# Performance work log

Hardware: AMD Instinct MI355X
Metric: run time of the kernel (lower is better)

The kernel has to match this reference:

```python
import jax, jax.numpy as jnp
import numpy as np

N_MELS = 80
FORMANT_START, FORMANT_END = 10, 50
W_L1, W_DELTA, W_DELTA2, W_SC, W_BAND, FORMANT_W = 1.0, 0.5, 0.25, 0.5, 1.0, 2.0
EPS = 1e-8


def _masked_mean(x, mask):
    # mask broadcasts to x's shape; count = sum of the broadcast mask
    n = jnp.maximum(jnp.sum(jnp.broadcast_to(mask, x.shape)), 1.0)
    return jnp.sum(x * mask) / n


def setup_inputs() -> dict:
    key = jax.random.key(0)
    k1, k2, k3 = jax.random.split(key, 3)
    B, T, D = 64, 4000, N_MELS
    pred_mel = jax.random.normal(k1, (B, T, D), dtype=jnp.float32)
    target_mel = jax.random.normal(k2, (B, T, D), dtype=jnp.float32)
    lengths = jax.random.randint(k3, (B,), T // 2, T + 1)
    mel_mask = (jnp.arange(T)[None, :] < lengths[:, None]).astype(jnp.float32)
    band_weights = jnp.ones((D,), dtype=jnp.float32).at[FORMANT_START:FORMANT_END].set(FORMANT_W)
    return {"pred_mel": pred_mel, "target_mel": target_mel, "mel_mask": mel_mask,
            "band_weights": band_weights}


def reference(pred_mel, target_mel, mel_mask, band_weights):
    mask3 = mel_mask[:, :, None]                      # (B,T,1)

    l1 = jnp.abs(pred_mel - target_mel)               # (B,T,D)
    l1_loss = _masked_mean(l1, mask3)

    # 1st-order deltas
    dp = pred_mel[:, 1:] - pred_mel[:, :-1]
    dt = target_mel[:, 1:] - target_mel[:, :-1]
    dmask = (mel_mask[:, 1:] * mel_mask[:, :-1])[:, :, None]
    delta_loss = _masked_mean(jnp.abs(dp - dt), dmask)

    # 2nd-order deltas
    d2p = dp[:, 1:] - dp[:, :-1]
    d2t = dt[:, 1:] - dt[:, :-1]
    d2mask = (mel_mask[:, 2:] * mel_mask[:, 1:-1] * mel_mask[:, :-2])[:, :, None]
    delta2_loss = _masked_mean(jnp.abs(d2p - d2t), d2mask)

    # spectral convergence
    diff = (pred_mel - target_mel) * mask3
    tgt_m = target_mel * mask3
    n = jnp.maximum(jnp.sum(jnp.broadcast_to(mask3, pred_mel.shape)), 1.0)
    sc_num = jnp.sqrt(jnp.sum(diff * diff) / n)
    sc_den = jnp.maximum(jnp.sqrt(jnp.sum(tgt_m * tgt_m) / n), EPS)
    sc_loss = sc_num / sc_den

    # band-weighted L1
    w = band_weights[None, None, :]
    band_loss = _masked_mean(l1 * w, mask3) / jnp.mean(band_weights)

    # energy (per-frame mean over mel bins)
    e_l1 = jnp.abs(pred_mel.mean(axis=-1) - target_mel.mean(axis=-1))  # (B,T)
    energy_loss = _masked_mean(e_l1, mel_mask)

    return (W_L1 * l1_loss + W_DELTA * delta_loss + W_DELTA2 * delta2_loss
            + W_SC * sc_loss + W_BAND * band_loss + 0.5 * energy_loss)
```

## Files before the change

### kernel.cpp

```cpp
#include <hip/hip_runtime.h>
#include <math.h>

#define D_MELS 80
#define T_DIM  4000
#define NQ     10
#define NTHR   256
#define RPI    14


__global__ __launch_bounds__(NTHR) void mel_loss_main(
    const float* __restrict__ pred, const float* __restrict__ tgt,
    const float* __restrict__ mask,
    float* __restrict__ partial, int BT, int Jtot, int K, int nblk)
{
    const int tid  = threadIdx.x;
    const int lane = tid & 63;
    const int qtr  = lane & 3;
    const int rw   = lane >> 2;
    const int gw   = blockIdx.x * (NTHR / 64) + (tid >> 6);

    const float4* p4 = (const float4*)pred;
    const float4* q4 = (const float4*)tgt;

    const int lsrc4 = (lane - 4) & 63;
    const int lsrc8 = (lane - 8) & 63;

    float4 sel0 = make_float4(0.f, 0.f, 0.f, 0.f);
    float4 sel3 = make_float4(0.f, 0.f, 0.f, 0.f);
    if (qtr == 2)      { sel0.z = 1.f; sel0.w = 1.f; }
    else if (qtr == 3) { sel0.x = 1.f; sel0.y = 1.f; sel0.z = 1.f; sel0.w = 1.f; }
    if (qtr == 0)      { sel3.x = 1.f; sel3.y = 1.f; }

    float v_l1 = 0.f, v_band = 0.f, v_diff2 = 0.f, v_tgt2 = 0.f, v_energy = 0.f;
    float v_m = 0.f, v_d = 0.f, v_dm = 0.f, v_d2 = 0.f, v_d2m = 0.f;

    const int j0 = gw * K;
    const int j1 = (j0 + K < Jtot) ? (j0 + K) : Jtot;

    for (int j = j0; j < j1; ++j) {
        const int r = j * RPI - 2 + rw;
        int rload = r;
        if (rload < 0) rload = 0;
        if (rload >= BT) rload = BT - 1;

        float mload = mask[rload];

        if (__any(mload != 0.0f)) {
            const int t = rload % T_DIM;

            const float4* pr = p4 + (size_t)rload * (D_MELS / 4) + qtr;
            const float4* qr = q4 + (size_t)rload * (D_MELS / 4) + qtr;

            float m1 = __shfl(mload, lsrc4, 64);
            float m2 = __shfl(mload, lsrc8, 64);

            const bool contrib = (rw >= 2) && (r < BT);
            float mt   = contrib ? mload : 0.f;
            float dmv  = (t >= 1) ? mt * m1 : 0.f;
            float d2mv = (t >= 2) ? dmv * m2 : 0.f;

            float l1r = 0.f, frr = 0.f, sqr = 0.f, t2r = 0.f, er = 0.f, dr = 0.f, d2r = 0.f;

            #pragma unroll
            for (int k = 0; k < 5; ++k) {
                float4 p = pr[4 * k];
                float4 q = qr[4 * k];
                float e0 = p.x - q.x, e1 = p.y - q.y, e2 = p.z - q.z, e3 = p.w - q.w;

                float f0 = __shfl(e0, lsrc4, 64);
                float f1 = __shfl(e1, lsrc4, 64);
                float f2 = __shfl(e2, lsrc4, 64);
                float f3 = __shfl(e3, lsrc4, 64);
                float g0 = __shfl(e0, lsrc8, 64);
                float g1 = __shfl(e1, lsrc8, 64);
                float g2 = __shfl(e2, lsrc8, 64);
                float g3 = __shfl(e3, lsrc8, 64);

                float a0 = fabsf(e0), a1 = fabsf(e1), a2 = fabsf(e2), a3 = fabsf(e3);
                float ak = a0 + a1 + a2 + a3;
                l1r += ak;
                if (k == 1 || k == 2)      frr += ak;
                else if (k == 0)           frr += a0 * sel0.x + a1 * sel0.y + a2 * sel0.z + a3 * sel0.w;
                else if (k == 3)           frr += a0 * sel3.x + a1 * sel3.y + a2 * sel3.z + a3 * sel3.w;

                sqr += e0 * e0 + e1 * e1 + e2 * e2 + e3 * e3;
                t2r += q.x * q.x + q.y * q.y + q.z * q.z + q.w * q.w;
                er  += e0 + e1 + e2 + e3;
                dr  += fabsf(e0 - f0) + fabsf(e1 - f1) + fabsf(e2 - f2) + fabsf(e3 - f3);
                d2r += fabsf(e0 - 2.f * f0 + g0) + fabsf(e1 - 2.f * f1 + g1)
                     + fabsf(e2 - 2.f * f2 + g2) + fabsf(e3 - 2.f * f3 + g3);
            }

            v_l1    += l1r * mt;
            v_band  += (l1r + frr) * mt;
            v_diff2 += sqr * mt;
            v_tgt2  += t2r * mt;
            v_d     += dr * dmv;
            v_d2    += d2r * d2mv;

            er += __shfl_xor(er, 1, 64);
            er += __shfl_xor(er, 2, 64);
            if (qtr == 0) {
                v_energy += fabsf(er) * mt;
                v_m   += mt;
                v_dm  += dmv;
                v_d2m += d2mv;
            }
        }
    }

    float vals[NQ] = {v_l1, v_band, v_diff2, v_tgt2, v_energy,
                      v_m, v_d, v_dm, v_d2, v_d2m};
    #pragma unroll
    for (int q = 0; q < NQ; ++q) {
        float v = vals[q];
        #pragma unroll
        for (int off = 32; off > 0; off >>= 1)
            v += __shfl_down(v, off, 64);
        vals[q] = v;
    }
    __shared__ float red[NTHR / 64][NQ];
    int wave = tid >> 6;
    if (lane == 0) {
        #pragma unroll
        for (int q = 0; q < NQ; ++q) red[wave][q] = vals[q];
    }
    __syncthreads();
    if (tid < NQ) {
        float s = 0.f;
        #pragma unroll
        for (int wv2 = 0; wv2 < NTHR / 64; ++wv2) s += red[wv2][tid];
        partial[tid * nblk + blockIdx.x] = s;
    }
}

__global__ __launch_bounds__(640) void mel_loss_finalize(
    const float* __restrict__ partial, const float* __restrict__ w,
    float* __restrict__ out, int nblk)
{
    const int tid = threadIdx.x;
    const int wv  = tid >> 6;
    const int lane = tid & 63;
    __shared__ float fin[NQ];

    float s = 0.f;
    for (int i = lane; i < nblk; i += 64) s += partial[wv * nblk + i];
    #pragma unroll
    for (int off = 32; off > 0; off >>= 1) s += __shfl_down(s, off, 64);
    if (lane == 0 && wv < NQ) fin[wv] = s;
    __syncthreads();

    if (tid == 0) {
        float l1s = fin[0], bands = fin[1], diff2 = fin[2], tgt2 = fin[3];
        float energys = fin[4], ms = fin[5], ds = fin[6], dms = fin[7];
        float d2s = fin[8], d2ms = fin[9];

        float wsum = 0.f;
        for (int d = 0; d < D_MELS; ++d) wsum += w[d];
        float wmean = wsum / (float)D_MELS;

        float n1  = fmaxf(ms   * (float)D_MELS, 1.f);
        float nd  = fmaxf(dms  * (float)D_MELS, 1.f);
        float nd2 = fmaxf(d2ms * (float)D_MELS, 1.f);

        float l1_loss     = l1s / n1;
        float delta_loss  = ds / nd;
        float delta2_loss = d2s / nd2;
        float sc_num = sqrtf(diff2 / n1);
        float sc_den = fmaxf(sqrtf(tgt2 / n1), 1e-8f);
        float sc_loss = sc_num / sc_den;
        float band_loss = (bands / n1) / wmean;
        float energy_loss = (energys / (float)D_MELS) / fmaxf(ms, 1.f);

        out[0] = 1.0f * l1_loss + 0.5f * delta_loss + 0.25f * delta2_loss
               + 0.5f * sc_loss + 1.0f * band_loss + 0.5f * energy_loss;
    }
}

extern "C" void kernel_launch(void* const* d_in, const int* in_sizes, int n_in,
                              void* d_out, int out_size, void* d_ws, size_t ws_size,
                              hipStream_t stream) {
    const float* pred = (const float*)d_in[0];
    const float* tgt  = (const float*)d_in[1];
    const float* mask = (const float*)d_in[2];
    const float* w    = (const float*)d_in[3];
    int BT = in_sizes[2];
    float* partial = (float*)d_ws;

    int Jtot = (BT + RPI - 1) / RPI;
    int K = 2;
    int nwaves = (Jtot + K - 1) / K;
    int grid = (nwaves + (NTHR / 64) - 1) / (NTHR / 64);
    while ((size_t)NQ * (size_t)grid * sizeof(float) > ws_size && K < Jtot) {
        K *= 2;
        nwaves = (Jtot + K - 1) / K;
        grid = (nwaves + (NTHR / 64) - 1) / (NTHR / 64);
    }

    mel_loss_main<<<grid, NTHR, 0, stream>>>(pred, tgt, mask, partial, BT, Jtot, K, grid);
    mel_loss_finalize<<<1, 640, 0, stream>>>(partial, w, (float*)d_out, grid);
}
```

Baseline: 189.6 us.

## Double-buffer row-group loads with compile-time tile count per wave

Each wave now processes a fixed six row-groups, with masks preloaded and two register buffers so the loads for group s+2 are issued while group s is computed. This is meant to hide global memory latency in the memory-bound reduction by keeping more loads in flight per wave. It raises register pressure and drops the workspace-size check that used to grow K when the partial buffer was too small, so a small workspace could overflow.

```diff
diff --git a/kernel.cpp b/kernel.cpp
--- a/kernel.cpp
+++ b/kernel.cpp
@@ -6,12 +6,13 @@
 #define NQ     10
 #define NTHR   256
 #define RPI    14
+#define KK     6
 
 
 __global__ __launch_bounds__(NTHR) void mel_loss_main(
     const float* __restrict__ pred, const float* __restrict__ tgt,
     const float* __restrict__ mask,
-    float* __restrict__ partial, int BT, int Jtot, int K, int nblk)
+    float* __restrict__ partial, int BT, int Jtot, int nblk)
 {
     const int tid  = threadIdx.x;
     const int lane = tid & 63;
@@ -21,90 +22,114 @@
 
     const float4* p4 = (const float4*)pred;
     const float4* q4 = (const float4*)tgt;
-
     const int lsrc4 = (lane - 4) & 63;
     const int lsrc8 = (lane - 8) & 63;
 
-    float4 sel0 = make_float4(0.f, 0.f, 0.f, 0.f);
-    float4 sel3 = make_float4(0.f, 0.f, 0.f, 0.f);
-    if (qtr == 2)      { sel0.z = 1.f; sel0.w = 1.f; }
-    else if (qtr == 3) { sel0.x = 1.f; sel0.y = 1.f; sel0.z = 1.f; sel0.w = 1.f; }
-    if (qtr == 0)      { sel3.x = 1.f; sel3.y = 1.f; }
-
     float v_l1 = 0.f, v_band = 0.f, v_diff2 = 0.f, v_tgt2 = 0.f, v_energy = 0.f;
     float v_m = 0.f, v_d = 0.f, v_dm = 0.f, v_d2 = 0.f, v_d2m = 0.f;
 
-    const int j0 = gw * K;
-    const int j1 = (j0 + K < Jtot) ? (j0 + K) : Jtot;
-
-    for (int j = j0; j < j1; ++j) {
-        const int r = j * RPI - 2 + rw;
-        int rload = r;
-        if (rload < 0) rload = 0;
-        if (rload >= BT) rload = BT - 1;
-
-        float mload = mask[rload];
-
-        if (__any(mload != 0.0f)) {
-            const int t = rload % T_DIM;
-
-            const float4* pr = p4 + (size_t)rload * (D_MELS / 4) + qtr;
-            const float4* qr = q4 + (size_t)rload * (D_MELS / 4) + qtr;
-
-            float m1 = __shfl(mload, lsrc4, 64);
-            float m2 = __shfl(mload, lsrc8, 64);
-
-            const bool contrib = (rw >= 2) && (r < BT);
-            float mt   = contrib ? mload : 0.f;
-            float dmv  = (t >= 1) ? mt * m1 : 0.f;
-            float d2mv = (t >= 2) ? dmv * m2 : 0.f;
-
-            float l1r = 0.f, frr = 0.f, sqr = 0.f, t2r = 0.f, er = 0.f, dr = 0.f, d2r = 0.f;
-
-            #pragma unroll
-            for (int k = 0; k < 5; ++k) {
-                float4 p = pr[4 * k];
-                float4 q = qr[4 * k];
-                float e0 = p.x - q.x, e1 = p.y - q.y, e2 = p.z - q.z, e3 = p.w - q.w;
-
-                float f0 = __shfl(e0, lsrc4, 64);
-                float f1 = __shfl(e1, lsrc4, 64);
-                float f2 = __shfl(e2, lsrc4, 64);
-                float f3 = __shfl(e3, lsrc4, 64);
-                float g0 = __shfl(e0, lsrc8, 64);
-                float g1 = __shfl(e1, lsrc8, 64);
-                float g2 = __shfl(e2, lsrc8, 64);
-                float g3 = __shfl(e3, lsrc8, 64);
-
-                float a0 = fabsf(e0), a1 = fabsf(e1), a2 = fabsf(e2), a3 = fabsf(e3);
-                float ak = a0 + a1 + a2 + a3;
-                l1r += ak;
-                if (k == 1 || k == 2)      frr += ak;
-                else if (k == 0)           frr += a0 * sel0.x + a1 * sel0.y + a2 * sel0.z + a3 * sel0.w;
-                else if (k == 3)           frr += a0 * sel3.x + a1 * sel3.y + a2 * sel3.z + a3 * sel3.w;
-
-                sqr += e0 * e0 + e1 * e1 + e2 * e2 + e3 * e3;
-                t2r += q.x * q.x + q.y * q.y + q.z * q.z + q.w * q.w;
-                er  += e0 + e1 + e2 + e3;
-                dr  += fabsf(e0 - f0) + fabsf(e1 - f1) + fabsf(e2 - f2) + fabsf(e3 - f3);
-                d2r += fabsf(e0 - 2.f * f0 + g0) + fabsf(e1 - 2.f * f1 + g1)
-                     + fabsf(e2 - 2.f * f2 + g2) + fabsf(e3 - 2.f * f3 + g3);
-            }
-
-            v_l1    += l1r * mt;
-            v_band  += (l1r + frr) * mt;
-            v_diff2 += sqr * mt;
-            v_tgt2  += t2r * mt;
-            v_d     += dr * dmv;
-            v_d2    += d2r * d2mv;
-
-            er += __shfl_xor(er, 1, 64);
-            er += __shfl_xor(er, 2, 64);
-            if (qtr == 0) {
-                v_energy += fabsf(er) * mt;
-                v_m   += mt;
-                v_dm  += dmv;
-                v_d2m += d2mv;
+    const int j0 = gw * KK;
+
+    auto laneRow = [&](int s) -> int {
+        int r = (j0 + s) * RPI - 2 + rw;
+        return r < 0 ? 0 : (r >= BT ? BT - 1 : r);
+    };
+
+    float mv[KK];
+    #pragma unroll
+    for (int s = 0; s < KK; ++s)
+        mv[s] = (j0 + s < Jtot) ? mask[laneRow(s)] : 0.f;
+
+    float4 PA[5], QA[5], PB[5], QB[5];
+
+    auto issueA = [&](int s) {
+        const int rload = laneRow(s);
+        const float4* pr = p4 + (size_t)rload * (D_MELS / 4) + qtr;
+        const float4* qr = q4 + (size_t)rload * (D_MELS / 4) + qtr;
+        #pragma unroll
+        for (int k = 0; k < 5; ++k) { PA[k] = pr[4 * k]; QA[k] = qr[4 * k]; }
+    };
+    auto issueB = [&](int s) {
+        const int rload = laneRow(s);
+        const float4* pr = p4 + (size_t)rload * (D_MELS / 4) + qtr;
+        const float4* qr = q4 + (size_t)rload * (D_MELS / 4) + qtr;
+        #pragma unroll
+        for (int k = 0; k < 5; ++k) { PB[k] = pr[4 * k]; QB[k] = qr[4 * k]; }
+    };
+
+    auto computeT = [&](const float4 (&P)[5], const float4 (&Q)[5], int s) {
+        const int r = (j0 + s) * RPI - 2 + rw;
+        const int rload = r < 0 ? 0 : (r >= BT ? BT - 1 : r);
+        const int t = rload % T_DIM;
+        const float mload = mv[s];
+        const float m1 = __shfl(mload, lsrc4, 64);
+        const float m2 = __shfl(mload, lsrc8, 64);
+        const bool contrib = (rw >= 2) && (r < BT);
+        const float mt   = contrib ? mload : 0.f;
+        const float dmv  = (t >= 1) ? mt * m1 : 0.f;
+        const float d2mv = (t >= 2) ? dmv * m2 : 0.f;
+
+        float l1r = 0.f, frr = 0.f, sqr = 0.f, t2r = 0.f, er = 0.f, dr = 0.f, d2r = 0.f;
+        #pragma unroll
+        for (int k = 0; k < 5; ++k) {
+            float4 p = P[k], q = Q[k];
+            float e0 = p.x - q.x, e1 = p.y - q.y, e2 = p.z - q.z, e3 = p.w - q.w;
+
+            float f0 = __shfl(e0, lsrc4, 64);
+            float f1 = __shfl(e1, lsrc4, 64);
+            float f2 = __shfl(e2, lsrc4, 64);
+            float f3 = __shfl(e3, lsrc4, 64);
+            float g0 = __shfl(e0, lsrc8, 64);
+            float g1 = __shfl(e1, lsrc8, 64);
+            float g2 = __shfl(e2, lsrc8, 64);
+            float g3 = __shfl(e3, lsrc8, 64);
+
+            float a0 = fabsf(e0), a1 = fabsf(e1), a2 = fabsf(e2), a3 = fabsf(e3);
+            float ak = a0 + a1 + a2 + a3;
+            l1r += ak;
+            if (k == 1 || k == 2) frr += ak;
+            else if (k == 0)      frr += (qtr == 2) ? (a2 + a3) : ((qtr == 3) ? ak : 0.f);
+            else if (k == 3)      frr += (qtr == 0) ? (a0 + a1) : 0.f;
+
+            sqr += e0 * e0 + e1 * e1 + e2 * e2 + e3 * e3;
+            t2r += q.x * q.x + q.y * q.y + q.z * q.z + q.w * q.w;
+            er  += e0 + e1 + e2 + e3;
+            dr  += fabsf(e0 - f0) + fabsf(e1 - f1) + fabsf(e2 - f2) + fabsf(e3 - f3);
+            d2r += fabsf(e0 - 2.f * f0 + g0) + fabsf(e1 - 2.f * f1 + g1)
+                 + fabsf(e2 - 2.f * f2 + g2) + fabsf(e3 - 2.f * f3 + g3);
+        }
+
+        v_l1    += l1r * mt;
+        v_band  += (l1r + frr) * mt;
+        v_diff2 += sqr * mt;
+        v_tgt2  += t2r * mt;
+        v_d     += dr * dmv;
+        v_d2    += d2r * d2mv;
+
+        er += __shfl_xor(er, 1, 64);
+        er += __shfl_xor(er, 2, 64);
+        if (qtr == 0) {
+            v_energy += fabsf(er) * mt;
+            v_m   += mt;
+            v_dm  += dmv;
+            v_d2m += d2mv;
+        }
+    };
+
+    issueA(0);
+    issueB(1);
+    #pragma unroll
+    for (int s = 0; s < KK; ++s) {
+        const bool liveS = __any(mv[s] != 0.f);
+        if (liveS) {
+            if ((s & 1) == 0) computeT(PA, QA, s);
+            else              computeT(PB, QB, s);
+        }
+        if (s + 2 < KK) {
+            const bool liveNN = __any(mv[s + 2] != 0.f);
+            if (liveNN) {
+                if ((s & 1) == 0) issueA(s + 2);
+                else              issueB(s + 2);
             }
         }
     }
@@ -188,15 +213,9 @@
     float* partial = (float*)d_ws;
 
     int Jtot = (BT + RPI - 1) / RPI;
-    int K = 2;
-    int nwaves = (Jtot + K - 1) / K;
+    int nwaves = (Jtot + KK - 1) / KK;
     int grid = (nwaves + (NTHR / 64) - 1) / (NTHR / 64);
-    while ((size_t)NQ * (size_t)grid * sizeof(float) > ws_size && K < Jtot) {
-        K *= 2;
-        nwaves = (Jtot + K - 1) / K;
-        grid = (nwaves + (NTHR / 64) - 1) / (NTHR / 64);
-    }
-
-    mel_loss_main<<<grid, NTHR, 0, stream>>>(pred, tgt, mask, partial, BT, Jtot, K, grid);
+
+    mel_loss_main<<<grid, NTHR, 0, stream>>>(pred, tgt, mask, partial, BT, Jtot, grid);
     mel_loss_finalize<<<1, 640, 0, stream>>>(partial, w, (float*)d_out, grid);
 }
```

After: 191.8 us. Within noise of the previous version (+1.1%).
